# Optimization experiments

Hardware: AMD Instinct MI355X
Metric: run time of the kernel (lower is better)

## Reference

```python
import jax, jax.numpy as jnp
import numpy as np
from jax import lax

T = 36          # sequence length
N_POLES = 80    # N -> dictionary has 2N+1 = 161 atoms
LAM = 0.1       # lam_f
MAX_ITER = 100
TOL = 1e-05


def real_D(T, rho, theta):
    # CONSTR=True: squash rho into [0.001, 1.15], theta into [0, pi]
    rmin, rmax = 0.001, 1.15
    r = rmin + (rmax - rmin) * jax.nn.sigmoid(rho)          # (N,)
    th = jnp.pi * jax.nn.sigmoid(theta)                     # (N,)
    i = jnp.arange(T, dtype=rho.dtype)[:, None]             # (T,1)
    p = r[None, :] ** i                                     # (T,N)
    W1 = p * jnp.cos(i * th[None, :])
    W2 = p * jnp.sin(i * th[None, :])
    D = jnp.concatenate([jnp.ones((T, 1), rho.dtype), W1, W2], axis=1)  # (T, 2N+1)
    # NORM=True: column-normalize all but the constant column
    norms = jnp.linalg.norm(D[:, 1:], axis=0, keepdims=True)
    return jnp.concatenate([D[:, :1], D[:, 1:] / norms], axis=1)


def softshrink(v, thr):
    return jnp.sign(v) * jnp.maximum(jnp.abs(v) - thr, 0.0)


def fista_efc(D, Y, lam, max_iter):
    # argmin_C ||Y - D C||_2^2 + lam |C|_1
    DtD = D.T @ D                                           # (P,P)
    L_inv = 1.0 / jnp.linalg.norm(DtD, ord=2)               # 1/spectral norm
    P = DtD.shape[0]
    dim_data = Y.shape[-1]
    A = jnp.eye(P, dtype=Y.dtype) - L_inv * DtD             # (P,P)
    B = L_inv * jnp.einsum('tp,btd->bpd', D, Y)             # (B,P,d)
    thr = lax.stop_gradient(lam * L_inv)                    # .item() in torch => constant

    batch = Y.shape[0]
    x0 = jnp.zeros((batch, P, dim_data), Y.dtype)
    y0 = jnp.zeros((batch, P, dim_data), Y.dtype)

    def body(carry, _):
        x, y, t, done = carry
        x_new = softshrink(jnp.einsum('pq,bqd->bpd', A, y) + B, thr)
        diff = jnp.linalg.norm(x - x_new) / dim_data        # Frobenius over all elems
        t_new = (1.0 + jnp.sqrt(1.0 + 4.0 * t * t)) / 2.0
        tt = (t - 1.0) / t_new
        y_new = (1.0 + tt) * x_new - tt * x
        # if already converged before this step, freeze the state (early return)
        x_out = jnp.where(done, x, x_new)
        y_out = jnp.where(done, y, y_new)
        t_out = jnp.where(done, t, t_new)
        done_new = done | (diff < TOL)
        return (x_out, y_out, t_out, done_new), None

    init = (x0, y0, jnp.float32(1.0), jnp.bool_(False))
    (x_fin, _, _, _), _ = lax.scan(body, init, None, length=max_iter)
    return x_fin


def reference(x, rho, theta):
    # DAN.forward with wiRH=False, freezeD=False
    dic = real_D(T, rho, theta)                             # (T, 2N+1)
    C = fista_efc(dic, x, LAM, MAX_ITER)                    # (B, 2N+1, d)
    reconst = jnp.einsum('tp,bpd->btd', dic, C)             # (B, T, d)
    return C, dic, reconst


def setup_inputs() -> dict:
    key = jax.random.key(0)
    k1, k2, k3 = jax.random.split(key, 3)
    x = jax.random.normal(k1, (256, T, 50), dtype=jnp.float32)
    rho = jax.random.uniform(k2, (N_POLES,), dtype=jnp.float32)
    theta = jax.random.uniform(k3, (N_POLES,), dtype=jnp.float32)
    return {"x": x, "rho": rho, "theta": theta}
```

## Files before the change

kernel.cpp:

```cpp
#include <hip/hip_runtime.h>
#include <math.h>

typedef _Float16 half_t;
typedef __attribute__((ext_vector_type(8))) _Float16 half8;
typedef __attribute__((ext_vector_type(4))) _Float16 half4;
typedef __attribute__((ext_vector_type(4))) float floatx4;

#define TDIM 36
#define PDIM 161
#define NCOL 50
#define NITER 100
#define PITER8 50

#define NKA 6
#define GSTR 44
#define SPS 196

#define YROW 384
#define RROW 128

#define SWZ(row, byteoff) ((byteoff) ^ (((row) & 7) << 4))

#define BY_Y    0
#define BY_R    24576
#define BY_LRTH 28672
#define BY_SC   32768
#define BY_GS   32784
#define BY_G2   39120
#define BY_G4   45456
#define LDS_TOTAL 51792

#define MFMA16 __builtin_amdgcn_mfma_f32_16x16x32_f16

__global__ __launch_bounds__(768, 3)
void dan_kernel(const float* __restrict__ xin, const float* __restrict__ rho,
                const float* __restrict__ theta, float* __restrict__ outC,
                float* __restrict__ outDic, float* __restrict__ outR)
{
  extern __shared__ char smc[];
  float*  sc   = (float*)(smc + BY_SC);
  float*  Gs   = (float*)(smc + BY_GS);
  float*  G2   = (float*)(smc + BY_G2);
  float*  G4   = (float*)(smc + BY_G4);
  float*  Df   = (float*)(smc + BY_Y);
  float*  lrth = (float*)(smc + BY_LRTH);

  const int tid = threadIdx.x;
  const int b = blockIdx.x;
  const int wave = tid >> 6, lane = tid & 63;
  const int q = lane >> 4, ln = lane & 15;

  {
    unsigned int* z = (unsigned int*)smc;
    for (int i = tid; i < LDS_TOTAL / 4; i += 768) z[i] = 0u;
  }
  __syncthreads();

  if (tid >= 1 && tid < PDIM) {
    const bool is_sin = tid > 80;
    const int n = is_sin ? (tid - 81) : (tid - 1);
    lrth[tid]       = logf(0.001f + 1.149f / (1.0f + expf(-rho[n])));
    lrth[161 + tid] = 3.14159265358979f / (1.0f + expf(-theta[n]));
  }
  __syncthreads();

  for (int i = tid; i < TDIM * PDIM; i += 768) {
    const int t = i / PDIM, p = i - t * PDIM;
    float val;
    if (p == 0) {
      val = 1.0f;
    } else {
      const float ft = (float)t;
      const float e = expf(ft * lrth[p]);
      const float ang = ft * lrth[161 + p];
      val = e * (p > 80 ? sinf(ang) : cosf(ang));
    }
    Df[t * SPS + p] = val;
  }
  __syncthreads();

  if (tid >= 1 && tid < PDIM) {
    float s2 = 0.0f;
    for (int t = 0; t < TDIM; ++t) {
      const float v = Df[t * SPS + tid];
      s2 += v * v;
    }
    const float inv = 1.0f / sqrtf(s2);
    for (int t = 0; t < TDIM; ++t) Df[t * SPS + tid] *= inv;
  }
  __syncthreads();

  if (tid < 666) {
    int i = 0, rem = tid;
    while (rem >= TDIM - i) { rem -= TDIM - i; ++i; }
    const int j = i + rem;
    const float4* ri = (const float4*)(Df + i * SPS);
    const float4* rj = (const float4*)(Df + j * SPS);
    float a = 0.0f;
    #pragma unroll 7
    for (int k = 0; k < SPS / 4; ++k) {
      const float4 x = ri[k], y = rj[k];
      a += x.x * y.x + x.y * y.y + x.z * y.z + x.w * y.w;
    }
    Gs[i * GSTR + j] = a;
    Gs[j * GSTR + i] = a;
  }
  if (b == 0) {
    for (int i = tid; i < TDIM * PDIM; i += 768) {
      const int t = i / PDIM, p = i - t * PDIM;
      outDic[i] = Df[t * SPS + p];
    }
  }

  const int mtA = wave >> 2;
  const int ntA = wave & 3;

  half8 DhF[NKA], DlF[NKA];
  {
    const int row = 16 * mtA + ln;
    #pragma unroll
    for (int ks = 0; ks < NKA; ++ks) {
      half8 hh = {0,0,0,0,0,0,0,0}, ll = {0,0,0,0,0,0,0,0};
      if (row < TDIM) {
        const float4 f0 = *(const float4*)(Df + row * SPS + 32 * ks + 8 * q);
        const float4 f1 = *(const float4*)(Df + row * SPS + 32 * ks + 8 * q + 4);
        const float fa[8] = {f0.x, f0.y, f0.z, f0.w, f1.x, f1.y, f1.z, f1.w};
        #pragma unroll
        for (int e = 0; e < 8; ++e) {
          const half_t h = (half_t)fa[e];
          hh[e] = h;
          ll[e] = (half_t)(fa[e] - (float)h);
        }
      }
      DhF[ks] = hh;
      DlF[ks] = ll;
    }
  }
  half8 DtH[2], DtL[2];
  if (wave < 11) {
    const int prow = 16 * wave + ln;
    #pragma unroll
    for (int ks = 0; ks < 2; ++ks) {
      half8 hh, ll;
      #pragma unroll
      for (int e = 0; e < 8; ++e) {
        const int t = 32 * ks + 8 * q + e;
        const float v = (t < TDIM) ? Df[t * SPS + prow] : 0.0f;
        const half_t h = (half_t)v;
        hh[e] = h;
        ll[e] = (half_t)(v - (float)h);
      }
      DtH[ks] = hh;
      DtL[ks] = ll;
    }
  }
  float yA[4];
  {
    const float* xb = xin + b * TDIM * NCOL;
    const int c = 16 * ntA + ln;
    #pragma unroll
    for (int r = 0; r < 4; ++r) {
      const int t = 16 * mtA + 4 * q + r;
      yA[r] = (t < TDIM && c < NCOL) ? xb[t * NCOL + c] : 0.0f;
    }
  }
  __syncthreads();

  if (tid < 666) {
    int i = 0, rem = tid;
    while (rem >= TDIM - i) { rem -= TDIM - i; ++i; }
    const int j = i + rem;
    const float4* ri = (const float4*)(Gs + i * GSTR);
    const float4* rj = (const float4*)(Gs + j * GSTR);
    float a = 0.0f;
    #pragma unroll
    for (int k = 0; k < GSTR / 4; ++k) {
      const float4 x = ri[k], y = rj[k];
      a += x.x * y.x + x.y * y.y + x.z * y.z + x.w * y.w;
    }
    G2[i * GSTR + j] = a;
    G2[j * GSTR + i] = a;
  }
  __syncthreads();
  if (tid < 666) {
    int i = 0, rem = tid;
    while (rem >= TDIM - i) { rem -= TDIM - i; ++i; }
    const int j = i + rem;
    const float4* ri = (const float4*)(G2 + i * GSTR);
    const float4* rj = (const float4*)(G2 + j * GSTR);
    float a = 0.0f;
    #pragma unroll
    for (int k = 0; k < GSTR / 4; ++k) {
      const float4 x = ri[k], y = rj[k];
      a += x.x * y.x + x.y * y.y + x.z * y.z + x.w * y.w;
    }
    G4[i * GSTR + j] = a;
    G4[j * GSTR + i] = a;
  }
  __syncthreads();
  if (tid < 666) {
    int i = 0, rem = tid;
    while (rem >= TDIM - i) { rem -= TDIM - i; ++i; }
    const int j = i + rem;
    const float4* ri = (const float4*)(G4 + i * GSTR);
    const float4* rj = (const float4*)(G4 + j * GSTR);
    float a = 0.0f;
    #pragma unroll
    for (int k = 0; k < GSTR / 4; ++k) {
      const float4 x = ri[k], y = rj[k];
      a += x.x * y.x + x.y * y.y + x.z * y.z + x.w * y.w;
    }
    G2[i * GSTR + j] = a;
    G2[j * GSTR + i] = a;
  }
  __syncthreads();

  if (wave == 0) {
    float g8r[36];
    #pragma unroll
    for (int j = 0; j < 36; ++j) g8r[j] = (lane < 36) ? G2[lane * GSTR + j] : 0.0f;
    float v = (lane < 36) ? 1.0f : 0.0f;
    for (int it = 0; it < PITER8; ++it) {
      const int vi = __float_as_int(v);
      float w0 = 0.0f, w1 = 0.0f, w2 = 0.0f, w3 = 0.0f;
      #pragma unroll
      for (int j = 0; j < 36; j += 4) {
        w0 = fmaf(g8r[j],     __int_as_float(__builtin_amdgcn_readlane(vi, j)),     w0);
        w1 = fmaf(g8r[j + 1], __int_as_float(__builtin_amdgcn_readlane(vi, j + 1)), w1);
        w2 = fmaf(g8r[j + 2], __int_as_float(__builtin_amdgcn_readlane(vi, j + 2)), w2);
        w3 = fmaf(g8r[j + 3], __int_as_float(__builtin_amdgcn_readlane(vi, j + 3)), w3);
      }
      float w = (w0 + w1) + (w2 + w3);
      float s = w * w;
      #pragma unroll
      for (int off = 32; off > 0; off >>= 1) s += __shfl_xor(s, off, 64);
      v = w * rsqrtf(s);
    }
    const int vi = __float_as_int(v);
    float w0 = 0.0f, w1 = 0.0f;
    #pragma unroll
    for (int j = 0; j < 36; j += 2) {
      const float gi0 = (lane < 36) ? Gs[lane * GSTR + j]     : 0.0f;
      const float gi1 = (lane < 36) ? Gs[lane * GSTR + j + 1] : 0.0f;
      w0 = fmaf(gi0, __int_as_float(__builtin_amdgcn_readlane(vi, j)),     w0);
      w1 = fmaf(gi1, __int_as_float(__builtin_amdgcn_readlane(vi, j + 1)), w1);
    }
    float num = v * (w0 + w1);
    #pragma unroll
    for (int off = 32; off > 0; off >>= 1) num += __shfl_xor(num, off, 64);
    if (lane == 0) {
      sc[0] = 1.0f / num;
      sc[1] = 0.1f / num;
    }
  } else {
    unsigned int* z = (unsigned int*)smc;
    for (int i = tid - 64; i < 32768 / 4; i += 704) z[i] = 0u;
  }
  __syncthreads();
  const float L_inv = sc[0];
  const float thr = sc[1];

  float xR[4][4], yR[4][4];
  #pragma unroll
  for (int nt = 0; nt < 4; ++nt)
    #pragma unroll
    for (int r = 0; r < 4; ++r) { xR[nt][r] = 0.0f; yR[nt][r] = 0.0f; }

  float tk = 1.0f;

  for (int it = 0; it < NITER; ++it) {
    {
      floatx4 aH0 = {0.f,0.f,0.f,0.f}, aH1 = {0.f,0.f,0.f,0.f};
      floatx4 aL0 = {0.f,0.f,0.f,0.f}, aL1 = {0.f,0.f,0.f,0.f};
      const int n0 = 16 * ntA + ln;
      const char* yrow = smc + BY_Y + n0 * YROW;
      #pragma unroll
      for (int ks = 0; ks < NKA; ++ks) {
        const int kb = (32 * ks + 8 * q) * 2;
        const half8 b0 = *(const half8*)(yrow + SWZ(n0, kb));
        if (ks & 1) {
          aH1 = MFMA16(DhF[ks], b0, aH1, 0, 0, 0);
          aL1 = MFMA16(DlF[ks], b0, aL1, 0, 0, 0);
        } else {
          aH0 = MFMA16(DhF[ks], b0, aH0, 0, 0, 0);
          aL0 = MFMA16(DlF[ks], b0, aL0, 0, 0, 0);
        }
      }
      const int t0 = 16 * mtA + 4 * q;
      half4 hv;
      #pragma unroll
      for (int r = 0; r < 4; ++r)
        hv[r] = (half_t)(yA[r] - ((aH0[r] + aH1[r]) + (aL0[r] + aL1[r])));
      *(half4*)(smc + BY_R + n0 * RROW + SWZ(n0, t0 * 2)) = hv;
    }
    __syncthreads();

    const float tnew = 0.5f * (1.0f + sqrtf(1.0f + 4.0f * tk * tk));
    const float ttf = (tk - 1.0f) / tnew;
    tk = tnew;

    if (wave < 11) {
      floatx4 acc[4];
      #pragma unroll
      for (int nt = 0; nt < 4; ++nt) {
        const int nr = 16 * nt + ln;
        const char* rrow = smc + BY_R + nr * RROW;
        const half8 rb0 = *(const half8*)(rrow + SWZ(nr, 16 * q));
        const half8 rb1 = *(const half8*)(rrow + SWZ(nr, 64 + 16 * q));
        floatx4 a = {0.f,0.f,0.f,0.f};
        a = MFMA16(DtH[0], rb0, a, 0, 0, 0);
        a = MFMA16(DtL[0], rb0, a, 0, 0, 0);
        a = MFMA16(DtH[1], rb1, a, 0, 0, 0);
        a = MFMA16(DtL[1], rb1, a, 0, 0, 0);
        acc[nt] = a;
      }
      const int p0 = 16 * wave + 4 * q;
      #pragma unroll
      for (int nt = 0; nt < 4; ++nt) {
        const int nr = 16 * nt + ln;
        half4 hv;
        #pragma unroll
        for (int r = 0; r < 4; ++r) {
          const float w = yR[nt][r] + L_inv * acc[nt][r];
          const float cl = fminf(fmaxf(w, -thr), thr);
          const float xn = w - cl;
          const float yn = xn + ttf * (xn - xR[nt][r]);
          xR[nt][r] = xn;
          yR[nt][r] = yn;
          hv[r] = (half_t)yn;
        }
        *(half4*)(smc + BY_Y + nr * YROW + SWZ(nr, p0 * 2)) = hv;
      }
    }
    __syncthreads();
  }

  float* Cb = outC + b * PDIM * NCOL;
  if (wave < 11) {
    #pragma unroll
    for (int nt = 0; nt < 4; ++nt) {
      const int c = 16 * nt + ln;
      if (c < NCOL) {
        #pragma unroll
        for (int r = 0; r < 4; ++r) {
          const int p = 16 * wave + 4 * q + r;
          if (p < PDIM) Cb[p * NCOL + c] = xR[nt][r];
        }
      }
    }
  }
  if (wave < 11) {
    const int p0 = 16 * wave + 4 * q;
    #pragma unroll
    for (int nt = 0; nt < 4; ++nt) {
      const int nr = 16 * nt + ln;
      half4 hv;
      #pragma unroll
      for (int r = 0; r < 4; ++r) hv[r] = (half_t)xR[nt][r];
      *(half4*)(smc + BY_Y + nr * YROW + SWZ(nr, p0 * 2)) = hv;
    }
  }
  __syncthreads();
  {
    floatx4 aH0 = {0.f,0.f,0.f,0.f}, aH1 = {0.f,0.f,0.f,0.f};
    floatx4 aL0 = {0.f,0.f,0.f,0.f}, aL1 = {0.f,0.f,0.f,0.f};
    const int n0 = 16 * ntA + ln;
    const char* yrow = smc + BY_Y + n0 * YROW;
    #pragma unroll
    for (int ks = 0; ks < NKA; ++ks) {
      const int kb = (32 * ks + 8 * q) * 2;
      const half8 b0 = *(const half8*)(yrow + SWZ(n0, kb));
      if (ks & 1) {
        aH1 = MFMA16(DhF[ks], b0, aH1, 0, 0, 0);
        aL1 = MFMA16(DlF[ks], b0, aL1, 0, 0, 0);
      } else {
        aH0 = MFMA16(DhF[ks], b0, aH0, 0, 0, 0);
        aL0 = MFMA16(DlF[ks], b0, aL0, 0, 0, 0);
      }
    }
    float* Rb = outR + b * TDIM * NCOL;
    const int c = 16 * ntA + ln;
    if (c < NCOL) {
      const int t0 = 16 * mtA + 4 * q;
      #pragma unroll
      for (int r = 0; r < 4; ++r) {
        const int t = t0 + r;
        if (t < TDIM) Rb[t * NCOL + c] = (aH0[r] + aH1[r]) + (aL0[r] + aL1[r]);
      }
    }
  }
}


extern "C" void kernel_launch(void* const* d_in, const int* in_sizes, int n_in,
                              void* d_out, int out_size, void* d_ws, size_t ws_size,
                              hipStream_t stream) {
  const float* x     = (const float*)d_in[0];
  const float* rho   = (const float*)d_in[1];
  const float* theta = (const float*)d_in[2];

  float* out    = (float*)d_out;
  float* outC   = out;
  float* outDic = out + 256 * PDIM * NCOL;
  float* outR   = outDic + TDIM * PDIM;

  hipLaunchKernelGGL(dan_kernel, dim3(256), dim3(768), LDS_TOTAL, stream,
                     x, rho, theta, outC, outDic, outR);
}
```

Before: 224.8 us.

## Split constant atom out and spread D^T R MFMA work across all twelve waves

The constant column of the dictionary is handled separately: its coefficient is updated with a scalar column-sum of the residual, stored in a small LDS slot, and subtracted or added as a bias. This lets the remaining 160 atoms fit in 5 K-slices, cutting one MFMA pair per wave in the D*Y step. The D^T*R step is redistributed so all 12 waves take part (3-4 atom tiles each) instead of 11 waves doing 4 column tiles each. The cost is more register-held D^T fragments per wave and some extra scalar shuffle work on one wave group.

```diff
diff --git a/kernel.cpp b/kernel.cpp
--- a/kernel.cpp
+++ b/kernel.cpp
@@ -12,7 +12,7 @@
 #define NITER 100
 #define PITER8 50
 
-#define NKA 6
+#define NKA 5
 #define GSTR 44
 #define SPS 196
 
@@ -24,11 +24,12 @@
 #define BY_Y    0
 #define BY_R    24576
 #define BY_LRTH 28672
-#define BY_SC   32768
-#define BY_GS   32784
-#define BY_G2   39120
-#define BY_G4   45456
-#define LDS_TOTAL 51792
+#define BY_Y0   32768
+#define BY_SC   33024
+#define BY_GS   33040
+#define BY_G2   39376
+#define BY_G4   45712
+#define LDS_TOTAL 52048
 
 #define MFMA16 __builtin_amdgcn_mfma_f32_16x16x32_f16
 
@@ -42,6 +43,7 @@
   float*  Gs   = (float*)(smc + BY_GS);
   float*  G2   = (float*)(smc + BY_G2);
   float*  G4   = (float*)(smc + BY_G4);
+  float*  Y0f  = (float*)(smc + BY_Y0);
   float*  Df   = (float*)(smc + BY_Y);
   float*  lrth = (float*)(smc + BY_LRTH);
 
@@ -114,44 +116,46 @@
 
   const int mtA = wave >> 2;
   const int ntA = wave & 3;
+  const int pgrp = wave >> 2;
+  const int npt = (pgrp == 0) ? 4 : 3;
 
   half8 DhF[NKA], DlF[NKA];
   {
     const int row = 16 * mtA + ln;
     #pragma unroll
     for (int ks = 0; ks < NKA; ++ks) {
-      half8 hh = {0,0,0,0,0,0,0,0}, ll = {0,0,0,0,0,0,0,0};
-      if (row < TDIM) {
-        const float4 f0 = *(const float4*)(Df + row * SPS + 32 * ks + 8 * q);
-        const float4 f1 = *(const float4*)(Df + row * SPS + 32 * ks + 8 * q + 4);
-        const float fa[8] = {f0.x, f0.y, f0.z, f0.w, f1.x, f1.y, f1.z, f1.w};
-        #pragma unroll
-        for (int e = 0; e < 8; ++e) {
-          const half_t h = (half_t)fa[e];
-          hh[e] = h;
-          ll[e] = (half_t)(fa[e] - (float)h);
-        }
-      }
-      DhF[ks] = hh;
-      DlF[ks] = ll;
-    }
-  }
-  half8 DtH[2], DtL[2];
-  if (wave < 11) {
-    const int prow = 16 * wave + ln;
-    #pragma unroll
-    for (int ks = 0; ks < 2; ++ks) {
       half8 hh, ll;
       #pragma unroll
       for (int e = 0; e < 8; ++e) {
-        const int t = 32 * ks + 8 * q + e;
-        const float v = (t < TDIM) ? Df[t * SPS + prow] : 0.0f;
+        const int p = 32 * ks + 8 * q + e + 1;
+        const float v = (row < TDIM) ? Df[row * SPS + p] : 0.0f;
         const half_t h = (half_t)v;
         hh[e] = h;
         ll[e] = (half_t)(v - (float)h);
       }
-      DtH[ks] = hh;
-      DtL[ks] = ll;
+      DhF[ks] = hh;
+      DlF[ks] = ll;
+    }
+  }
+  half8 DtH[4][2], DtL[4][2];
+  #pragma unroll
+  for (int k = 0; k < 4; ++k) {
+    if (k < npt) {
+      const int atom = 16 * (pgrp + 3 * k) + ln + 1;
+      #pragma unroll
+      for (int ks = 0; ks < 2; ++ks) {
+        half8 hh, ll;
+        #pragma unroll
+        for (int e = 0; e < 8; ++e) {
+          const int t = 32 * ks + 8 * q + e;
+          const float v = (t < TDIM) ? Df[t * SPS + atom] : 0.0f;
+          const half_t h = (half_t)v;
+          hh[e] = h;
+          ll[e] = (half_t)(v - (float)h);
+        }
+        DtH[k][ks] = hh;
+        DtL[k][ks] = ll;
+      }
     }
   }
   float yA[4];
@@ -254,7 +258,7 @@
     }
   } else {
     unsigned int* z = (unsigned int*)smc;
-    for (int i = tid - 64; i < 32768 / 4; i += 704) z[i] = 0u;
+    for (int i = tid - 64; i < BY_SC / 4; i += 704) z[i] = 0u;
   }
   __syncthreads();
   const float L_inv = sc[0];
@@ -262,17 +266,19 @@
 
   float xR[4][4], yR[4][4];
   #pragma unroll
-  for (int nt = 0; nt < 4; ++nt)
-    #pragma unroll
-    for (int r = 0; r < 4; ++r) { xR[nt][r] = 0.0f; yR[nt][r] = 0.0f; }
+  for (int k = 0; k < 4; ++k)
+    #pragma unroll
+    for (int r = 0; r < 4; ++r) { xR[k][r] = 0.0f; yR[k][r] = 0.0f; }
+  float x0v = 0.0f, y0v = 0.0f;
 
   float tk = 1.0f;
 
   for (int it = 0; it < NITER; ++it) {
     {
+      const int n0 = 16 * ntA + ln;
+      const float y0c = Y0f[n0];
       floatx4 aH0 = {0.f,0.f,0.f,0.f}, aH1 = {0.f,0.f,0.f,0.f};
       floatx4 aL0 = {0.f,0.f,0.f,0.f}, aL1 = {0.f,0.f,0.f,0.f};
-      const int n0 = 16 * ntA + ln;
       const char* yrow = smc + BY_Y + n0 * YROW;
       #pragma unroll
       for (int ks = 0; ks < NKA; ++ks) {
@@ -290,7 +296,7 @@
       half4 hv;
       #pragma unroll
       for (int r = 0; r < 4; ++r)
-        hv[r] = (half_t)(yA[r] - ((aH0[r] + aH1[r]) + (aL0[r] + aL1[r])));
+        hv[r] = (half_t)(yA[r] - y0c - ((aH0[r] + aH1[r]) + (aL0[r] + aL1[r])));
       *(half4*)(smc + BY_R + n0 * RROW + SWZ(n0, t0 * 2)) = hv;
     }
     __syncthreads();
@@ -299,72 +305,94 @@
     const float ttf = (tk - 1.0f) / tnew;
     tk = tnew;
 
-    if (wave < 11) {
-      floatx4 acc[4];
-      #pragma unroll
-      for (int nt = 0; nt < 4; ++nt) {
-        const int nr = 16 * nt + ln;
-        const char* rrow = smc + BY_R + nr * RROW;
-        const half8 rb0 = *(const half8*)(rrow + SWZ(nr, 16 * q));
-        const half8 rb1 = *(const half8*)(rrow + SWZ(nr, 64 + 16 * q));
-        floatx4 a = {0.f,0.f,0.f,0.f};
-        a = MFMA16(DtH[0], rb0, a, 0, 0, 0);
-        a = MFMA16(DtL[0], rb0, a, 0, 0, 0);
-        a = MFMA16(DtH[1], rb1, a, 0, 0, 0);
-        a = MFMA16(DtL[1], rb1, a, 0, 0, 0);
-        acc[nt] = a;
-      }
-      const int p0 = 16 * wave + 4 * q;
-      #pragma unroll
-      for (int nt = 0; nt < 4; ++nt) {
-        const int nr = 16 * nt + ln;
+    {
+      const int c = 16 * ntA + ln;
+      const char* rrow = smc + BY_R + c * RROW;
+      const half8 rb0 = *(const half8*)(rrow + SWZ(c, 16 * q));
+      const half8 rb1 = *(const half8*)(rrow + SWZ(c, 64 + 16 * q));
+
+      if (pgrp == 1) {
+        float s0 = 0.0f;
+        #pragma unroll
+        for (int e = 0; e < 8; ++e) s0 += (float)rb0[e];
+        float s1 = 0.0f;
+        #pragma unroll
+        for (int e = 0; e < 4; ++e) s1 += (float)rb1[e];
+        float part = s0 + (q == 0 ? s1 : 0.0f);
+        part += __shfl_xor(part, 16, 64);
+        part += __shfl_xor(part, 32, 64);
+        const float w = y0v + L_inv * part;
+        const float cl = fminf(fmaxf(w, -thr), thr);
+        const float xn = w - cl;
+        const float yn = xn + ttf * (xn - x0v);
+        x0v = xn;
+        y0v = yn;
+        if (q == 0) Y0f[c] = yn;
+      }
+
+      #pragma unroll
+      for (int k = 0; k < 4; ++k) {
+        if (k < npt) {
+          floatx4 a = {0.f,0.f,0.f,0.f};
+          a = MFMA16(DtH[k][0], rb0, a, 0, 0, 0);
+          a = MFMA16(DtL[k][0], rb0, a, 0, 0, 0);
+          a = MFMA16(DtH[k][1], rb1, a, 0, 0, 0);
+          a = MFMA16(DtL[k][1], rb1, a, 0, 0, 0);
+          const int s0_ = 16 * (pgrp + 3 * k) + 4 * q;
+          half4 hv;
+          #pragma unroll
+          for (int r = 0; r < 4; ++r) {
+            const float w = yR[k][r] + L_inv * a[r];
+            const float cl = fminf(fmaxf(w, -thr), thr);
+            const float xn = w - cl;
+            const float yn = xn + ttf * (xn - xR[k][r]);
+            xR[k][r] = xn;
+            yR[k][r] = yn;
+            hv[r] = (half_t)yn;
+          }
+          *(half4*)(smc + BY_Y + c * YROW + SWZ(c, s0_ * 2)) = hv;
+        }
+      }
+    }
+    __syncthreads();
+  }
+
+  float* Cb = outC + b * PDIM * NCOL;
+  {
+    const int c = 16 * ntA + ln;
+    if (c < NCOL) {
+      #pragma unroll
+      for (int k = 0; k < 4; ++k) {
+        if (k < npt) {
+          const int pbase = 16 * (pgrp + 3 * k) + 4 * q + 1;
+          #pragma unroll
+          for (int r = 0; r < 4; ++r)
+            Cb[(pbase + r) * NCOL + c] = xR[k][r];
+        }
+      }
+      if (pgrp == 1 && q == 0) Cb[c] = x0v;
+    }
+  }
+  {
+    const int c = 16 * ntA + ln;
+    #pragma unroll
+    for (int k = 0; k < 4; ++k) {
+      if (k < npt) {
+        const int s0_ = 16 * (pgrp + 3 * k) + 4 * q;
         half4 hv;
         #pragma unroll
-        for (int r = 0; r < 4; ++r) {
-          const float w = yR[nt][r] + L_inv * acc[nt][r];
-          const float cl = fminf(fmaxf(w, -thr), thr);
-          const float xn = w - cl;
-          const float yn = xn + ttf * (xn - xR[nt][r]);
-          xR[nt][r] = xn;
-          yR[nt][r] = yn;
-          hv[r] = (half_t)yn;
-        }
-        *(half4*)(smc + BY_Y + nr * YROW + SWZ(nr, p0 * 2)) = hv;
-      }
-    }
-    __syncthreads();
-  }
-
-  float* Cb = outC + b * PDIM * NCOL;
-  if (wave < 11) {
-    #pragma unroll
-    for (int nt = 0; nt < 4; ++nt) {
-      const int c = 16 * nt + ln;
-      if (c < NCOL) {
-        #pragma unroll
-        for (int r = 0; r < 4; ++r) {
-          const int p = 16 * wave + 4 * q + r;
-          if (p < PDIM) Cb[p * NCOL + c] = xR[nt][r];
-        }
-      }
-    }
-  }
-  if (wave < 11) {
-    const int p0 = 16 * wave + 4 * q;
-    #pragma unroll
-    for (int nt = 0; nt < 4; ++nt) {
-      const int nr = 16 * nt + ln;
-      half4 hv;
-      #pragma unroll
-      for (int r = 0; r < 4; ++r) hv[r] = (half_t)xR[nt][r];
-      *(half4*)(smc + BY_Y + nr * YROW + SWZ(nr, p0 * 2)) = hv;
-    }
-  }
-  __syncthreads();
-  {
+        for (int r = 0; r < 4; ++r) hv[r] = (half_t)xR[k][r];
+        *(half4*)(smc + BY_Y + c * YROW + SWZ(c, s0_ * 2)) = hv;
+      }
+    }
+    if (pgrp == 1 && q == 0) Y0f[c] = x0v;
+  }
+  __syncthreads();
+  {
+    const int n0 = 16 * ntA + ln;
+    const float x0c = Y0f[n0];
     floatx4 aH0 = {0.f,0.f,0.f,0.f}, aH1 = {0.f,0.f,0.f,0.f};
     floatx4 aL0 = {0.f,0.f,0.f,0.f}, aL1 = {0.f,0.f,0.f,0.f};
-    const int n0 = 16 * ntA + ln;
     const char* yrow = smc + BY_Y + n0 * YROW;
     #pragma unroll
     for (int ks = 0; ks < NKA; ++ks) {
@@ -379,13 +407,14 @@
       }
     }
     float* Rb = outR + b * TDIM * NCOL;
-    const int c = 16 * ntA + ln;
+    const int c = n0;
     if (c < NCOL) {
       const int t0 = 16 * mtA + 4 * q;
       #pragma unroll
       for (int r = 0; r < 4; ++r) {
         const int t = t0 + r;
-        if (t < TDIM) Rb[t * NCOL + c] = (aH0[r] + aH1[r]) + (aL0[r] + aL1[r]);
+        if (t < TDIM)
+          Rb[t * NCOL + c] = x0c + (aH0[r] + aH1[r]) + (aL0[r] + aL1[r]);
       }
     }
   }
```

After: 239.3 us. 6.5% more time.

## Give each wave its own column tile to remove per-iteration block barriers

Applied to the files above, without the earlier changes.

The work split changes from 12 waves tiling a T×N / P×N grid to 4 waves, each owning 16 columns across all rows. Every wave then computes its own residual and FISTA update, so the two __syncthreads per iteration are no longer needed. The fp16 hi/lo dictionary fragments move from registers into swizzled LDS arrays. The transposed path now uses only the high half, which drops the low-order correction in D^T r. This trades barrier cost for fewer waves per block, more LDS traffic per MFMA, more LDS per block, and lower accuracy in that product.

```diff
diff --git a/kernel.cpp b/kernel.cpp
--- a/kernel.cpp
+++ b/kernel.cpp
@@ -18,6 +18,8 @@
 
 #define YROW 384
 #define RROW 128
+#define DROW 384
+#define TROW 128
 
 #define SWZ(row, byteoff) ((byteoff) ^ (((row) & 7) << 4))
 
@@ -25,14 +27,17 @@
 #define BY_R    24576
 #define BY_LRTH 28672
 #define BY_SC   32768
-#define BY_GS   32784
-#define BY_G2   39120
-#define BY_G4   45456
-#define LDS_TOTAL 51792
+#define BY_DAH  32784
+#define BY_DAL  51216
+#define BY_DTH  69648
+#define BY_GS   92176
+#define BY_G2   98512
+#define BY_G4   104848
+#define LDS_TOTAL 111184
 
 #define MFMA16 __builtin_amdgcn_mfma_f32_16x16x32_f16
 
-__global__ __launch_bounds__(768, 3)
+__global__ __launch_bounds__(256, 1)
 void dan_kernel(const float* __restrict__ xin, const float* __restrict__ rho,
                 const float* __restrict__ theta, float* __restrict__ outC,
                 float* __restrict__ outDic, float* __restrict__ outR)
@@ -49,10 +54,11 @@
   const int b = blockIdx.x;
   const int wave = tid >> 6, lane = tid & 63;
   const int q = lane >> 4, ln = lane & 15;
+  const int col = 16 * wave + ln;
 
   {
     unsigned int* z = (unsigned int*)smc;
-    for (int i = tid; i < LDS_TOTAL / 4; i += 768) z[i] = 0u;
+    for (int i = tid; i < LDS_TOTAL / 4; i += 256) z[i] = 0u;
   }
   __syncthreads();
 
@@ -64,7 +70,7 @@
   }
   __syncthreads();
 
-  for (int i = tid; i < TDIM * PDIM; i += 768) {
+  for (int i = tid; i < TDIM * PDIM; i += 256) {
     const int t = i / PDIM, p = i - t * PDIM;
     float val;
     if (p == 0) {
@@ -90,8 +96,8 @@
   }
   __syncthreads();
 
-  if (tid < 666) {
-    int i = 0, rem = tid;
+  for (int job = tid; job < 666; job += 256) {
+    int i = 0, rem = job;
     while (rem >= TDIM - i) { rem -= TDIM - i; ++i; }
     const int j = i + rem;
     const float4* ri = (const float4*)(Df + i * SPS);
@@ -105,69 +111,32 @@
     Gs[i * GSTR + j] = a;
     Gs[j * GSTR + i] = a;
   }
-  if (b == 0) {
-    for (int i = tid; i < TDIM * PDIM; i += 768) {
-      const int t = i / PDIM, p = i - t * PDIM;
-      outDic[i] = Df[t * SPS + p];
-    }
-  }
-
-  const int mtA = wave >> 2;
-  const int ntA = wave & 3;
-
-  half8 DhF[NKA], DlF[NKA];
-  {
-    const int row = 16 * mtA + ln;
-    #pragma unroll
-    for (int ks = 0; ks < NKA; ++ks) {
-      half8 hh = {0,0,0,0,0,0,0,0}, ll = {0,0,0,0,0,0,0,0};
-      if (row < TDIM) {
-        const float4 f0 = *(const float4*)(Df + row * SPS + 32 * ks + 8 * q);
-        const float4 f1 = *(const float4*)(Df + row * SPS + 32 * ks + 8 * q + 4);
-        const float fa[8] = {f0.x, f0.y, f0.z, f0.w, f1.x, f1.y, f1.z, f1.w};
-        #pragma unroll
-        for (int e = 0; e < 8; ++e) {
-          const half_t h = (half_t)fa[e];
-          hh[e] = h;
-          ll[e] = (half_t)(fa[e] - (float)h);
-        }
-      }
-      DhF[ks] = hh;
-      DlF[ks] = ll;
-    }
-  }
-  half8 DtH[2], DtL[2];
-  if (wave < 11) {
-    const int prow = 16 * wave + ln;
-    #pragma unroll
-    for (int ks = 0; ks < 2; ++ks) {
-      half8 hh, ll;
-      #pragma unroll
-      for (int e = 0; e < 8; ++e) {
-        const int t = 32 * ks + 8 * q + e;
-        const float v = (t < TDIM) ? Df[t * SPS + prow] : 0.0f;
-        const half_t h = (half_t)v;
-        hh[e] = h;
-        ll[e] = (half_t)(v - (float)h);
-      }
-      DtH[ks] = hh;
-      DtL[ks] = ll;
-    }
-  }
-  float yA[4];
+  for (int i = tid; i < TDIM * PDIM; i += 256) {
+    const int t = i / PDIM, p = i - t * PDIM;
+    const float v = Df[t * SPS + p];
+    const half_t h = (half_t)v;
+    const half_t l = (half_t)(v - (float)h);
+    *(half_t*)(smc + BY_DAH + t * DROW + SWZ(t, p * 2)) = h;
+    *(half_t*)(smc + BY_DAL + t * DROW + SWZ(t, p * 2)) = l;
+    *(half_t*)(smc + BY_DTH + p * TROW + SWZ(p, t * 2)) = h;
+    if (b == 0) outDic[i] = v;
+  }
+  float yA[3][4];
   {
     const float* xb = xin + b * TDIM * NCOL;
-    const int c = 16 * ntA + ln;
-    #pragma unroll
-    for (int r = 0; r < 4; ++r) {
-      const int t = 16 * mtA + 4 * q + r;
-      yA[r] = (t < TDIM && c < NCOL) ? xb[t * NCOL + c] : 0.0f;
-    }
-  }
-  __syncthreads();
-
-  if (tid < 666) {
-    int i = 0, rem = tid;
+    #pragma unroll
+    for (int mt = 0; mt < 3; ++mt) {
+      #pragma unroll
+      for (int r = 0; r < 4; ++r) {
+        const int t = 16 * mt + 4 * q + r;
+        yA[mt][r] = (t < TDIM && col < NCOL) ? xb[t * NCOL + col] : 0.0f;
+      }
+    }
+  }
+  __syncthreads();
+
+  for (int job = tid; job < 666; job += 256) {
+    int i = 0, rem = job;
     while (rem >= TDIM - i) { rem -= TDIM - i; ++i; }
     const int j = i + rem;
     const float4* ri = (const float4*)(Gs + i * GSTR);
@@ -182,8 +151,8 @@
     G2[j * GSTR + i] = a;
   }
   __syncthreads();
-  if (tid < 666) {
-    int i = 0, rem = tid;
+  for (int job = tid; job < 666; job += 256) {
+    int i = 0, rem = job;
     while (rem >= TDIM - i) { rem -= TDIM - i; ++i; }
     const int j = i + rem;
     const float4* ri = (const float4*)(G2 + i * GSTR);
@@ -198,8 +167,8 @@
     G4[j * GSTR + i] = a;
   }
   __syncthreads();
-  if (tid < 666) {
-    int i = 0, rem = tid;
+  for (int job = tid; job < 666; job += 256) {
+    int i = 0, rem = job;
     while (rem >= TDIM - i) { rem -= TDIM - i; ++i; }
     const int j = i + rem;
     const float4* ri = (const float4*)(G4 + i * GSTR);
@@ -254,138 +223,129 @@
     }
   } else {
     unsigned int* z = (unsigned int*)smc;
-    for (int i = tid - 64; i < 32768 / 4; i += 704) z[i] = 0u;
+    for (int i = tid - 64; i < (BY_R + 8192) / 4; i += 192) z[i] = 0u;
   }
   __syncthreads();
   const float L_inv = sc[0];
   const float thr = sc[1];
 
-  float xR[4][4], yR[4][4];
+  float xS[11][4], yS[11][4];
   #pragma unroll
-  for (int nt = 0; nt < 4; ++nt)
-    #pragma unroll
-    for (int r = 0; r < 4; ++r) { xR[nt][r] = 0.0f; yR[nt][r] = 0.0f; }
+  for (int pt = 0; pt < 11; ++pt)
+    #pragma unroll
+    for (int r = 0; r < 4; ++r) { xS[pt][r] = 0.0f; yS[pt][r] = 0.0f; }
 
   float tk = 1.0f;
 
   for (int it = 0; it < NITER; ++it) {
+    half8 yb[NKA];
     {
-      floatx4 aH0 = {0.f,0.f,0.f,0.f}, aH1 = {0.f,0.f,0.f,0.f};
-      floatx4 aL0 = {0.f,0.f,0.f,0.f}, aL1 = {0.f,0.f,0.f,0.f};
-      const int n0 = 16 * ntA + ln;
-      const char* yrow = smc + BY_Y + n0 * YROW;
+      const char* yrow = smc + BY_Y + col * YROW;
+      #pragma unroll
+      for (int ks = 0; ks < NKA; ++ks)
+        yb[ks] = *(const half8*)(yrow + SWZ(col, (32 * ks + 8 * q) * 2));
+    }
+    #pragma unroll
+    for (int mt = 0; mt < 3; ++mt) {
+      const int row = 16 * mt + ln;
+      const char* dah = smc + BY_DAH + row * DROW;
+      const char* dal = smc + BY_DAL + row * DROW;
+      floatx4 aH = {0.f,0.f,0.f,0.f}, aL = {0.f,0.f,0.f,0.f};
       #pragma unroll
       for (int ks = 0; ks < NKA; ++ks) {
         const int kb = (32 * ks + 8 * q) * 2;
-        const half8 b0 = *(const half8*)(yrow + SWZ(n0, kb));
-        if (ks & 1) {
-          aH1 = MFMA16(DhF[ks], b0, aH1, 0, 0, 0);
-          aL1 = MFMA16(DlF[ks], b0, aL1, 0, 0, 0);
-        } else {
-          aH0 = MFMA16(DhF[ks], b0, aH0, 0, 0, 0);
-          aL0 = MFMA16(DlF[ks], b0, aL0, 0, 0, 0);
-        }
-      }
-      const int t0 = 16 * mtA + 4 * q;
+        const half8 ah = *(const half8*)(dah + SWZ(row, kb));
+        const half8 al = *(const half8*)(dal + SWZ(row, kb));
+        aH = MFMA16(ah, yb[ks], aH, 0, 0, 0);
+        aL = MFMA16(al, yb[ks], aL, 0, 0, 0);
+      }
+      const int t0 = 16 * mt + 4 * q;
       half4 hv;
       #pragma unroll
       for (int r = 0; r < 4; ++r)
-        hv[r] = (half_t)(yA[r] - ((aH0[r] + aH1[r]) + (aL0[r] + aL1[r])));
-      *(half4*)(smc + BY_R + n0 * RROW + SWZ(n0, t0 * 2)) = hv;
-    }
-    __syncthreads();
+        hv[r] = (half_t)(yA[mt][r] - (aH[r] + aL[r]));
+      *(half4*)(smc + BY_R + col * RROW + SWZ(col, t0 * 2)) = hv;
+    }
 
     const float tnew = 0.5f * (1.0f + sqrtf(1.0f + 4.0f * tk * tk));
     const float ttf = (tk - 1.0f) / tnew;
     tk = tnew;
 
-    if (wave < 11) {
-      floatx4 acc[4];
-      #pragma unroll
-      for (int nt = 0; nt < 4; ++nt) {
-        const int nr = 16 * nt + ln;
-        const char* rrow = smc + BY_R + nr * RROW;
-        const half8 rb0 = *(const half8*)(rrow + SWZ(nr, 16 * q));
-        const half8 rb1 = *(const half8*)(rrow + SWZ(nr, 64 + 16 * q));
+    {
+      const char* rrow = smc + BY_R + col * RROW;
+      const half8 rb0 = *(const half8*)(rrow + SWZ(col, (8 * q) * 2));
+      const half8 rb1 = *(const half8*)(rrow + SWZ(col, (32 + 8 * q) * 2));
+      #pragma unroll
+      for (int pt = 0; pt < 11; ++pt) {
+        const int rowT = 16 * pt + ln;
+        const char* th = smc + BY_DTH + rowT * TROW;
         floatx4 a = {0.f,0.f,0.f,0.f};
-        a = MFMA16(DtH[0], rb0, a, 0, 0, 0);
-        a = MFMA16(DtL[0], rb0, a, 0, 0, 0);
-        a = MFMA16(DtH[1], rb1, a, 0, 0, 0);
-        a = MFMA16(DtL[1], rb1, a, 0, 0, 0);
-        acc[nt] = a;
-      }
-      const int p0 = 16 * wave + 4 * q;
-      #pragma unroll
-      for (int nt = 0; nt < 4; ++nt) {
-        const int nr = 16 * nt + ln;
+        a = MFMA16(*(const half8*)(th + SWZ(rowT, (8 * q) * 2)),        rb0, a, 0, 0, 0);
+        a = MFMA16(*(const half8*)(th + SWZ(rowT, (32 + 8 * q) * 2)),   rb1, a, 0, 0, 0);
+        const int p0 = 16 * pt + 4 * q;
         half4 hv;
         #pragma unroll
         for (int r = 0; r < 4; ++r) {
-          const float w = yR[nt][r] + L_inv * acc[nt][r];
+          const float w = yS[pt][r] + L_inv * a[r];
           const float cl = fminf(fmaxf(w, -thr), thr);
           const float xn = w - cl;
-          const float yn = xn + ttf * (xn - xR[nt][r]);
-          xR[nt][r] = xn;
-          yR[nt][r] = yn;
+          const float yn = xn + ttf * (xn - xS[pt][r]);
+          xS[pt][r] = xn;
+          yS[pt][r] = yn;
           hv[r] = (half_t)yn;
         }
-        *(half4*)(smc + BY_Y + nr * YROW + SWZ(nr, p0 * 2)) = hv;
-      }
-    }
-    __syncthreads();
+        *(half4*)(smc + BY_Y + col * YROW + SWZ(col, p0 * 2)) = hv;
+      }
+    }
   }
 
   float* Cb = outC + b * PDIM * NCOL;
-  if (wave < 11) {
-    #pragma unroll
-    for (int nt = 0; nt < 4; ++nt) {
-      const int c = 16 * nt + ln;
-      if (c < NCOL) {
+  if (col < NCOL) {
+    #pragma unroll
+    for (int pt = 0; pt < 11; ++pt) {
+      #pragma unroll
+      for (int r = 0; r < 4; ++r) {
+        const int p = 16 * pt + 4 * q + r;
+        if (p < PDIM) Cb[p * NCOL + col] = xS[pt][r];
+      }
+    }
+  }
+  #pragma unroll
+  for (int pt = 0; pt < 11; ++pt) {
+    const int p0 = 16 * pt + 4 * q;
+    half4 hv;
+    #pragma unroll
+    for (int r = 0; r < 4; ++r) hv[r] = (half_t)xS[pt][r];
+    *(half4*)(smc + BY_Y + col * YROW + SWZ(col, p0 * 2)) = hv;
+  }
+  {
+    half8 xb8[NKA];
+    const char* yrow = smc + BY_Y + col * YROW;
+    #pragma unroll
+    for (int ks = 0; ks < NKA; ++ks)
+      xb8[ks] = *(const half8*)(yrow + SWZ(col, (32 * ks + 8 * q) * 2));
+    float* Rb = outR + b * TDIM * NCOL;
+    #pragma unroll
+    for (int mt = 0; mt < 3; ++mt) {
+      const int row = 16 * mt + ln;
+      const char* dah = smc + BY_DAH + row * DROW;
+      const char* dal = smc + BY_DAL + row * DROW;
+      floatx4 aH = {0.f,0.f,0.f,0.f}, aL = {0.f,0.f,0.f,0.f};
+      #pragma unroll
+      for (int ks = 0; ks < NKA; ++ks) {
+        const int kb = (32 * ks + 8 * q) * 2;
+        const half8 ah = *(const half8*)(dah + SWZ(row, kb));
+        const half8 al = *(const half8*)(dal + SWZ(row, kb));
+        aH = MFMA16(ah, xb8[ks], aH, 0, 0, 0);
+        aL = MFMA16(al, xb8[ks], aL, 0, 0, 0);
+      }
+      if (col < NCOL) {
+        const int t0 = 16 * mt + 4 * q;
         #pragma unroll
         for (int r = 0; r < 4; ++r) {
-          const int p = 16 * wave + 4 * q + r;
-          if (p < PDIM) Cb[p * NCOL + c] = xR[nt][r];
+          const int t = t0 + r;
+          if (t < TDIM) Rb[t * NCOL + col] = aH[r] + aL[r];
         }
-      }
-    }
-  }
-  if (wave < 11) {
-    const int p0 = 16 * wave + 4 * q;
-    #pragma unroll
-    for (int nt = 0; nt < 4; ++nt) {
-      const int nr = 16 * nt + ln;
-      half4 hv;
-      #pragma unroll
-      for (int r = 0; r < 4; ++r) hv[r] = (half_t)xR[nt][r];
-      *(half4*)(smc + BY_Y + nr * YROW + SWZ(nr, p0 * 2)) = hv;
-    }
-  }
-  __syncthreads();
-  {
-    floatx4 aH0 = {0.f,0.f,0.f,0.f}, aH1 = {0.f,0.f,0.f,0.f};
-    floatx4 aL0 = {0.f,0.f,0.f,0.f}, aL1 = {0.f,0.f,0.f,0.f};
-    const int n0 = 16 * ntA + ln;
-    const char* yrow = smc + BY_Y + n0 * YROW;
-    #pragma unroll
-    for (int ks = 0; ks < NKA; ++ks) {
-      const int kb = (32 * ks + 8 * q) * 2;
-      const half8 b0 = *(const half8*)(yrow + SWZ(n0, kb));
-      if (ks & 1) {
-        aH1 = MFMA16(DhF[ks], b0, aH1, 0, 0, 0);
-        aL1 = MFMA16(DlF[ks], b0, aL1, 0, 0, 0);
-      } else {
-        aH0 = MFMA16(DhF[ks], b0, aH0, 0, 0, 0);
-        aL0 = MFMA16(DlF[ks], b0, aL0, 0, 0, 0);
-      }
-    }
-    float* Rb = outR + b * TDIM * NCOL;
-    const int c = 16 * ntA + ln;
-    if (c < NCOL) {
-      const int t0 = 16 * mtA + 4 * q;
-      #pragma unroll
-      for (int r = 0; r < 4; ++r) {
-        const int t = t0 + r;
-        if (t < TDIM) Rb[t * NCOL + c] = (aH0[r] + aH1[r]) + (aL0[r] + aL1[r]);
       }
     }
   }
@@ -404,6 +364,6 @@
   float* outDic = out + 256 * PDIM * NCOL;
   float* outR   = outDic + TDIM * PDIM;
 
-  hipLaunchKernelGGL(dan_kernel, dim3(256), dim3(768), LDS_TOTAL, stream,
+  hipLaunchKernelGGL(dan_kernel, dim3(256), dim3(256), LDS_TOTAL, stream,
                      x, rho, theta, outC, outDic, outR);
 }
```

Result: slower. 290.5 us (+29.2%).
